# Performance work log

Hardware: AMD Instinct MI355X
Metric: run time of the kernel (lower is better)

## Reference

```python
import jax, jax.numpy as jnp
import numpy as np

NEG_SLOPE = 0.01  # F.leaky_relu default
FGW = 0.1         # feature_guidance_weight


def gat_layer(x, src, dst, W, att_l, att_r, heads, out_ch, concat):
    N = x.shape[0]
    # reward-based guidance weights (L1-normalized over nodes, F.normalize p=1 dim=0)
    rw = 1.0 / (jnp.abs(x[:, -1:]) + 1e-6)                    # [N,1]
    rw = rw / jnp.maximum(jnp.sum(jnp.abs(rw), axis=0), 1e-12)
    h = (x @ W).reshape(N, heads, out_ch)                      # [N,H,C]
    # per-node attention halves, gathered per edge (avoids [E,H,C] for scores)
    al = jnp.sum(h * att_l, axis=-1)                           # [N,H] (x_i side)
    ar = jnp.sum(h * att_r, axis=-1)                           # [N,H] (x_j side)
    alpha = jax.nn.leaky_relu(al[dst] + ar[src], NEG_SLOPE)    # [E,H]
    alpha = alpha + FGW * jnp.log(rw[src])                     # guidance from source node
    # segment softmax over incoming edges of each target node (PyG softmax)
    m = jax.ops.segment_max(alpha, dst, num_segments=N)        # [N,H]
    e = jnp.exp(alpha - m[dst])
    s = jax.ops.segment_sum(e, dst, num_segments=N)
    alpha = e / (s[dst] + 1e-16)                               # [E,H]
    # weighted scatter-aggregate of source features
    msg = h[src] * alpha[:, :, None]                           # [E,H,C]
    out = jax.ops.segment_sum(msg, dst, num_segments=N)        # [N,H,C]
    if concat:
        return out.reshape(N, heads * out_ch)
    return out.mean(axis=1)


def setup_inputs() -> dict:
    key = jax.random.key(0)
    ks = jax.random.split(key, 10)
    N, E, D_IN, HID, HEADS, D_OUT = 50000, 800000, 128, 64, 4, 1

    def xavier(k, shape, fan_in, fan_out):
        a = jnp.sqrt(6.0 / (fan_in + fan_out))
        return jax.random.uniform(k, shape, jnp.float32, -a, a)

    x = jax.random.normal(ks[0], (N, D_IN), jnp.float32)
    edge_index = jax.random.randint(ks[1], (2, E), 0, N, jnp.int32)
    W1 = xavier(ks[2], (D_IN, HEADS * HID), D_IN, HEADS * HID)
    att_l1 = xavier(ks[3], (1, HEADS, HID), HID, HID)
    att_r1 = xavier(ks[4], (1, HEADS, HID), HID, HID)
    W2 = xavier(ks[5], (HEADS * HID, HID), HEADS * HID, HID)
    att_l2 = xavier(ks[6], (1, 1, HID), HID, HID)
    att_r2 = xavier(ks[7], (1, 1, HID), HID, HID)
    fc_w = xavier(ks[8], (HID, D_OUT), HID, D_OUT)
    fc_b = jnp.zeros((D_OUT,), jnp.float32)
    return {"x": x, "edge_index": edge_index, "W1": W1, "att_l1": att_l1,
            "att_r1": att_r1, "W2": W2, "att_l2": att_l2, "att_r2": att_r2,
            "fc_w": fc_w, "fc_b": fc_b}


def reference(x, edge_index, W1, att_l1, att_r1, W2, att_l2, att_r2, fc_w, fc_b):
    src, dst = edge_index[0], edge_index[1]
    HID, HEADS = 64, 4
    h = gat_layer(x, src, dst, W1, att_l1, att_r1, HEADS, HID, concat=True)
    h = jax.nn.elu(h)  # dropout omitted (eval mode)
    h = gat_layer(h, src, dst, W2, att_l2, att_r2, 1, HID, concat=False)
    h = jax.nn.elu(h)
    return h @ fc_w + fc_b
```

## Files before the change

kernel.cpp:

```cpp
#include <hip/hip_runtime.h>
#include <hip/hip_bf16.h>

typedef __hip_bfloat16 bf16;
typedef __attribute__((ext_vector_type(8))) short bf16x8;
typedef __attribute__((ext_vector_type(4))) float f32x4;

#define NEG_SLOPE 0.01f
#define FGW 0.1f

__device__ __forceinline__ float b2f(bf16 v) { return __bfloat162float(v); }

__device__ __forceinline__ float ldf(const void* p, size_t i, int isbf) {
    return isbf ? b2f(((const bf16*)p)[i]) : ((const float*)p)[i];
}

__device__ __forceinline__ float bu2f(unsigned short u) {
    return __uint_as_float(((unsigned)u) << 16);
}
__device__ __forceinline__ unsigned short f2bu(float f) {
    return __bfloat16_as_ushort(__float2bfloat16(f));
}

__device__ __forceinline__ float waveReduceSum(float v) {
#pragma unroll
    for (int o = 32; o > 0; o >>= 1) v += __shfl_down(v, o, 64);
    return v;
}

#define ATOMIC_ADD_F32(p, v) unsafeAtomicAdd((p), (v))

__global__ __launch_bounds__(256) void k_degdet(const int* __restrict__ ei, int* __restrict__ deg, int E,
                                                const unsigned short* __restrict__ xr,
                                                float* __restrict__ sscal, int* __restrict__ flag,
                                                const void* __restrict__ W1, const void* __restrict__ W2,
                                                unsigned short* __restrict__ Wp1h,
                                                unsigned short* __restrict__ Wp1l,
                                                unsigned short* __restrict__ Wp2) {
    __shared__ int sflag;
    const int t = threadIdx.x;
    const bool packer = (blockIdx.x < 128);
    if (packer) {
        if (t < 64) {
            int big = 0;
            for (int i = t; i < 256; i += 64) {
                int ex = (xr[i] >> 7) & 0xFF;
                if (ex >= 0xBF) big = 1;
            }
            unsigned long long mk = __ballot(big);
            if (t == 0) sflag = (mk == 0ull) ? 1 : 0;
        }
        __syncthreads();
        const int isbf = sflag;
        if (blockIdx.x == 0 && t == 0) {
            *flag = isbf;
            sscal[0] = 0.f; sscal[1] = 0.f;
        }
        int id = blockIdx.x * 256 + t;
        {
            int j = id & 7, l = (id >> 3) & 63, ko = (id >> 9) & 3, T = id >> 11;
            int k = ko * 32 + (l >> 4) * 8 + j, col = T * 16 + (l & 15);
            float wv = ldf(W1, (size_t)k * 256 + col, isbf);
            unsigned short hi = f2bu(wv);
            Wp1h[id] = hi;
            Wp1l[id] = f2bu(wv - bu2f(hi));
        }
        if (id < 16384) {
            int j = id & 7, l = (id >> 3) & 63, ko = (id >> 9) & 7, T = id >> 12;
            int k = ko * 32 + (l >> 4) * 8 + j, col = T * 16 + (l & 15);
            Wp2[id] = f2bu(ldf(W2, (size_t)k * 64 + col, isbf));
        }
    }
    int e = blockIdx.x * 256 + t;
    if (e < E) atomicAdd(&deg[ei[E + e]], 1);
}

__global__ __launch_bounds__(256) void k_scanA(const int* __restrict__ deg, int* __restrict__ tmp,
                                               int* __restrict__ bsum, int N) {
    __shared__ int part[256];
    const int t = threadIdx.x;
    int i = blockIdx.x * 256 + t;
    int v = (i < N) ? ((deg[i] + 3) & ~3) : 0;
    part[t] = v;
    __syncthreads();
    for (int o = 1; o < 256; o <<= 1) {
        int add = (t >= o) ? part[t - o] : 0;
        __syncthreads();
        part[t] += add;
        __syncthreads();
    }
    if (i < N) tmp[i] = part[t];
    if (t == 255) bsum[blockIdx.x] = part[255];
}

__global__ __launch_bounds__(256) void k_scanB(int* __restrict__ bsum, int nb, int* __restrict__ rowptrN) {
    __shared__ int part[256];
    const int t = threadIdx.x;
    const int K = (nb + 255) / 256;
    int vs[8];
    int lsum = 0;
#pragma unroll
    for (int k = 0; k < 8; k++) {
        int idx = t * K + k;
        vs[k] = (k < K && idx < nb) ? bsum[idx] : 0;
        lsum += vs[k];
    }
    part[t] = lsum;
    __syncthreads();
    for (int o = 1; o < 256; o <<= 1) {
        int add = (t >= o) ? part[t - o] : 0;
        __syncthreads();
        part[t] += add;
        __syncthreads();
    }
    int excl = part[t] - lsum;
#pragma unroll
    for (int k = 0; k < 8; k++) {
        int idx = t * K + k;
        if (k < K && idx < nb) { bsum[idx] = excl; excl += vs[k]; }
    }
    if (t == 255) *rowptrN = part[255];
}

__global__ __launch_bounds__(256) void k_scanC(const int* __restrict__ deg, const int* __restrict__ tmp,
                                               const int* __restrict__ bsum, int* __restrict__ rowptr,
                                               int* __restrict__ cursor, int* __restrict__ csr_src, int N) {
    int i = blockIdx.x * 256 + threadIdx.x;
    if (i >= N) return;
    int dg = deg[i];
    int pd = (dg + 3) & ~3;
    int base = bsum[blockIdx.x] + tmp[i] - pd;
    rowptr[i] = base;
    cursor[i] = 0;
    for (int j = dg; j < pd; j++) csr_src[base + j] = N;
}

__global__ __launch_bounds__(256) void k_scatter(const int* __restrict__ ei, const int* __restrict__ rowptr,
                                                 int* __restrict__ cursor, int* __restrict__ csr_src, int E) {
    int e = blockIdx.x * 256 + threadIdx.x;
    if (e >= E) return;
    int d = ei[E + e];
    int pos = atomicAdd(&cursor[d], 1);
    csr_src[rowptr[d] + pos] = ei[e];
}

__global__ __launch_bounds__(256) void k_gemm1f(const void* __restrict__ x,
                                                const unsigned short* __restrict__ Wp1h,
                                                const unsigned short* __restrict__ Wp1l,
                                                const void* __restrict__ attl,
                                                const void* __restrict__ attr,
                                                unsigned short* __restrict__ h1,
                                                float* __restrict__ pk1,
                                                float* __restrict__ al1,
                                                float* __restrict__ rwS,
                                                int N, const int* __restrict__ flag) {
    const int isbf = *flag;
    __shared__ unsigned short Ash[64 * 136];
    __shared__ unsigned short Asl[64 * 136];
    __shared__ float rpart[64];
    const int row0 = blockIdx.x * 64;
    const int t = threadIdx.x;
    const int w = t >> 6, lane = t & 63;
    const int m = lane & 15, quad = lane >> 4;

    if (blockIdx.x == 0) {
        if (t < 32) *reinterpret_cast<uint4*>(&h1[(size_t)N * 256 + t * 8]) = (uint4){0u, 0u, 0u, 0u};
        if (t < 8) pk1[(size_t)N * 8 + t] = (t < 4) ? -1e30f : 0.f;
    }

#pragma unroll
    for (int it = 0; it < 4; it++) {
        int idx = it * 256 + t;
        int r = idx >> 4, c = idx & 15;
        if (isbf) {
            uint4 raw = {0u, 0u, 0u, 0u};
            if (row0 + r < N) {
                const unsigned short* xu = (const unsigned short*)x;
                raw = *reinterpret_cast<const uint4*>(xu + (size_t)(row0 + r) * 128 + c * 8);
            }
            *reinterpret_cast<uint4*>(&Ash[r * 136 + c * 8]) = raw;
        } else {
            float v[8];
            if (row0 + r < N) {
                const float* xf = (const float*)x;
                float4 a = *reinterpret_cast<const float4*>(xf + (size_t)(row0 + r) * 128 + c * 8);
                float4 b = *reinterpret_cast<const float4*>(xf + (size_t)(row0 + r) * 128 + c * 8 + 4);
                v[0] = a.x; v[1] = a.y; v[2] = a.z; v[3] = a.w;
                v[4] = b.x; v[5] = b.y; v[6] = b.z; v[7] = b.w;
            } else {
#pragma unroll
                for (int k = 0; k < 8; k++) v[k] = 0.f;
            }
            unsigned short hi[8], lo[8];
#pragma unroll
            for (int k = 0; k < 8; k++) {
                hi[k] = f2bu(v[k]);
                lo[k] = f2bu(v[k] - bu2f(hi[k]));
            }
            *reinterpret_cast<uint4*>(&Ash[r * 136 + c * 8]) = *reinterpret_cast<const uint4*>(hi);
            *reinterpret_cast<uint4*>(&Asl[r * 136 + c * 8]) = *reinterpret_cast<const uint4*>(lo);
        }
    }
    __syncthreads();

    bf16x8 Bh[4][4];
#pragma unroll
    for (int tt = 0; tt < 4; tt++)
#pragma unroll
        for (int ko = 0; ko < 4; ko++)
            Bh[tt][ko] = *reinterpret_cast<const bf16x8*>(
                &Wp1h[(size_t)(((w * 4 + tt) * 4 + ko) * 64 + lane) * 8]);
    float avl[4], avr[4];
#pragma unroll
    for (int tt = 0; tt < 4; tt++) {
        int col = (w * 4 + tt) * 16 + m;
        avl[tt] = ldf(attl, col, isbf);
        avr[tt] = ldf(attr, col, isbf);
    }
    for (int sub = 0; sub < 4; sub++) {
        const int rbase = sub * 16;
        bf16x8 Ah[4];
#pragma unroll
        for (int ko = 0; ko < 4; ko++)
            Ah[ko] = *reinterpret_cast<const bf16x8*>(&Ash[(rbase + m) * 136 + ko * 32 + quad * 8]);
        f32x4 Cf[4];
#pragma unroll
        for (int tt = 0; tt < 4; tt++) Cf[tt] = (f32x4){0.f, 0.f, 0.f, 0.f};
        if (isbf) {
#pragma unroll
            for (int ko = 0; ko < 4; ko++)
#pragma unroll
                for (int tt = 0; tt < 4; tt++)
                    Cf[tt] = __builtin_amdgcn_mfma_f32_16x16x32_bf16(Ah[ko], Bh[tt][ko], Cf[tt], 0, 0, 0);
        } else {
            bf16x8 Al[4];
#pragma unroll
            for (int ko = 0; ko < 4; ko++)
                Al[ko] = *reinterpret_cast<const bf16x8*>(&Asl[(rbase + m) * 136 + ko * 32 + quad * 8]);
#pragma unroll
            for (int ko = 0; ko < 4; ko++)
#pragma unroll
                for (int tt = 0; tt < 4; tt++) {
                    Cf[tt] = __builtin_amdgcn_mfma_f32_16x16x32_bf16(Ah[ko], Bh[tt][ko], Cf[tt], 0, 0, 0);
                    Cf[tt] = __builtin_amdgcn_mfma_f32_16x16x32_bf16(Al[ko], Bh[tt][ko], Cf[tt], 0, 0, 0);
                    bf16x8 Bl = *reinterpret_cast<const bf16x8*>(
                        &Wp1l[(size_t)(((w * 4 + tt) * 4 + ko) * 64 + lane) * 8]);
                    Cf[tt] = __builtin_amdgcn_mfma_f32_16x16x32_bf16(Ah[ko], Bl, Cf[tt], 0, 0, 0);
                }
        }
#pragma unroll
        for (int tt = 0; tt < 4; tt++) {
            int col = (w * 4 + tt) * 16 + m;
#pragma unroll
            for (int reg = 0; reg < 4; reg++) {
                int row = row0 + rbase + quad * 4 + reg;
                if (row < N) h1[(size_t)row * 256 + col] = f2bu(Cf[tt][reg]);
            }
        }
        if (w == 3 && m == 15) {
#pragma unroll
            for (int reg = 0; reg < 4; reg++) {
                int row = row0 + rbase + quad * 4 + reg;
                if (row < N) pk1[(size_t)row * 8 + 5] = Cf[3][reg];
            }
        }
        float sl[4], sr[4];
#pragma unroll
        for (int reg = 0; reg < 4; reg++) {
            float a = 0.f, b = 0.f;
#pragma unroll
            for (int tt = 0; tt < 4; tt++) {
                a = fmaf(avl[tt], Cf[tt][reg], a);
                b = fmaf(avr[tt], Cf[tt][reg], b);
            }
            sl[reg] = a; sr[reg] = b;
        }
#pragma unroll
        for (int off = 8; off >= 1; off >>= 1) {
#pragma unroll
            for (int reg = 0; reg < 4; reg++) {
                sl[reg] += __shfl_down(sl[reg], off, 64);
                sr[reg] += __shfl_down(sr[reg], off, 64);
            }
        }
        if (m == 0) {
#pragma unroll
            for (int reg = 0; reg < 4; reg++) {
                int row = row0 + rbase + quad * 4 + reg;
                if (row < N) {
                    al1[(size_t)row * 4 + w] = sl[reg];
                    pk1[(size_t)row * 8 + w] = sr[reg];
                }
            }
        }
    }
    if (t < 64) {
        int row = row0 + t;
        float rr = 0.f;
        if (row < N) {
            float a = fabsf(ldf(x, (size_t)row * 128 + 127, isbf));
            rr = 1.f / (a + 1e-6f);
            pk1[(size_t)row * 8 + 4] = logf(rr);
        }
        rpart[t] = rr;
    }
    __syncthreads();
    if (t == 0) {
        float s = 0.f;
#pragma unroll
        for (int i = 0; i < 64; i++) s += rpart[i];
        ATOMIC_ADD_F32(rwS, s);
    }
}

__global__ __launch_bounds__(256) void k_agg1(const int* __restrict__ rowptr,
                                              const int* __restrict__ csr_src,
                                              const float* __restrict__ al1,
                                              const float* __restrict__ pk1,
                                              const float* __restrict__ rwS,
                                              const unsigned short* __restrict__ h1,
                                              unsigned short* __restrict__ x2b,
                                              float* __restrict__ x2c, int N) {
    const int d = blockIdx.x * 4 + (threadIdx.x >> 6);
    if (d >= N) return;
    const int lane = threadIdx.x & 63;
    const int q = lane & 15;
    const int g = lane >> 4;
    const int h = q >> 2;
    const bool last15 = (q == 15);
    const float gl = FGW * logf(fmaxf(*rwS, 1e-12f));
    const unsigned qo = (unsigned)q * 32u;
    const unsigned ho4 = (unsigned)h * 4u;
    const char* pk1c = (const char*)pk1;
    const char* h1c  = (const char*)h1;

    const float al_h = al1[(size_t)d * 4 + h];
    const int beg = rowptr[d], end = rowptr[d + 1];

    float acc[16];
#pragma unroll
    for (int k = 0; k < 16; k++) acc[k] = 0.f;
    float ssum = 0.f;

    for (int base = beg; base < end; base += 32) {
        const int nst = min(end - base, 32) >> 2;

        int sj[8];
#pragma unroll
        for (int k = 0; k < 8; k++)
            if (k < nst) sj[k] = csr_src[base + k * 4 + g];

        float arP[6]; float2 lcP[6]; uint4 h0P[6], h1P[6];

#define LD1(K) do {                                                                   \
        int s_ = sj[(K)];                                                             \
        unsigned po_ = (unsigned)s_ * 32u;                                            \
        arP[(K) % 6] = *reinterpret_cast<const float*>(pk1c + po_ + ho4);             \
        lcP[(K) % 6] = *reinterpret_cast<const float2*>(pk1c + po_ + 16u);            \
        unsigned ho_ = (unsigned)s_ * 512u + qo;                                      \
        h0P[(K) % 6] = *reinterpret_cast<const uint4*>(h1c + ho_);                    \
        h1P[(K) % 6] = *reinterpret_cast<const uint4*>(h1c + ho_ + 16u);              \
    } while (0)

#define CONS1(K) do {                                                                 \
        float a_ = al_h + arP[(K) % 6];                                               \
        a_ = fmaxf(a_, NEG_SLOPE * a_);                                               \
        a_ = fmaf(FGW, lcP[(K) % 6].x, a_ - gl);                                      \
        float e_ = __expf(a_);                                                        \
        ssum += e_;                                                                   \
        uint4 cb0_ = h0P[(K) % 6], cb1_ = h1P[(K) % 6];                               \
        unsigned uu_; float lo_, hi_;                                                 \
        uu_ = cb0_.x; lo_ = __uint_as_float(uu_ << 16); hi_ = __uint_as_float(uu_ & 0xFFFF0000u); \
        acc[0] = fmaf(e_, lo_, acc[0]);  acc[1] = fmaf(e_, hi_, acc[1]);              \
        uu_ = cb0_.y; lo_ = __uint_as_float(uu_ << 16); hi_ = __uint_as_float(uu_ & 0xFFFF0000u); \
        acc[2] = fmaf(e_, lo_, acc[2]);  acc[3] = fmaf(e_, hi_, acc[3]);              \
        uu_ = cb0_.z; lo_ = __uint_as_float(uu_ << 16); hi_ = __uint_as_float(uu_ & 0xFFFF0000u); \
        acc[4] = fmaf(e_, lo_, acc[4]);  acc[5] = fmaf(e_, hi_, acc[5]);              \
        uu_ = cb0_.w; lo_ = __uint_as_float(uu_ << 16); hi_ = __uint_as_float(uu_ & 0xFFFF0000u); \
        acc[6] = fmaf(e_, lo_, acc[6]);  acc[7] = fmaf(e_, hi_, acc[7]);              \
        uu_ = cb1_.x; lo_ = __uint_as_float(uu_ << 16); hi_ = __uint_as_float(uu_ & 0xFFFF0000u); \
        acc[8] = fmaf(e_, lo_, acc[8]);  acc[9] = fmaf(e_, hi_, acc[9]);              \
        uu_ = cb1_.y; lo_ = __uint_as_float(uu_ << 16); hi_ = __uint_as_float(uu_ & 0xFFFF0000u); \
        acc[10] = fmaf(e_, lo_, acc[10]); acc[11] = fmaf(e_, hi_, acc[11]);           \
        uu_ = cb1_.z; lo_ = __uint_as_float(uu_ << 16); hi_ = __uint_as_float(uu_ & 0xFFFF0000u); \
        acc[12] = fmaf(e_, lo_, acc[12]); acc[13] = fmaf(e_, hi_, acc[13]);           \
        uu_ = cb1_.w; lo_ = __uint_as_float(uu_ << 16); hi_ = __uint_as_float(uu_ & 0xFFFF0000u); \
        hi_ = last15 ? lcP[(K) % 6].y : hi_;    \
        acc[14] = fmaf(e_, lo_, acc[14]); acc[15] = fmaf(e_, hi_, acc[15]);           \
    } while (0)

        LD1(0);
        if (1 < nst) LD1(1);
        if (2 < nst) LD1(2);
        if (3 < nst) LD1(3);
        if (4 < nst) LD1(4);
#pragma unroll
        for (int k = 0; k < 8; k++) {
            if (k >= nst) break;
            if (k + 5 < 8) { if (k + 5 < nst) LD1(k + 5); }
            CONS1(k);
        }
#undef LD1
#undef CONS1
    }

#pragma unroll
    for (int k = 0; k < 16; k++) {
        acc[k] += __shfl_xor(acc[k], 16, 64);
        acc[k] += __shfl_xor(acc[k], 32, 64);
    }
    ssum += __shfl_xor(ssum, 16, 64);
    ssum += __shfl_xor(ssum, 32, 64);

    const float inv = 1.f / (ssum + 1e-16f);
    float o0 = (g == 0 ? acc[0] : g == 1 ? acc[4]  : g == 2 ? acc[8]  : acc[12]);
    float o1 = (g == 0 ? acc[1] : g == 1 ? acc[5]  : g == 2 ? acc[9]  : acc[13]);
    float o2 = (g == 0 ? acc[2] : g == 1 ? acc[6]  : g == 2 ? acc[10] : acc[14]);
    float o3 = (g == 0 ? acc[3] : g == 1 ? acc[7]  : g == 2 ? acc[11] : acc[15]);
    o0 *= inv; o1 *= inv; o2 *= inv; o3 *= inv;
    o0 = (o0 > 0.f) ? o0 : expm1f(o0);
    o1 = (o1 > 0.f) ? o1 : expm1f(o1);
    o2 = (o2 > 0.f) ? o2 : expm1f(o2);
    o3 = (o3 > 0.f) ? o3 : expm1f(o3);
    uint2 ob;
    ob.x = (unsigned)f2bu(o0) | ((unsigned)f2bu(o1) << 16);
    ob.y = (unsigned)f2bu(o2) | ((unsigned)f2bu(o3) << 16);
    *reinterpret_cast<uint2*>(&x2b[(size_t)d * 256 + q * 16 + g * 4]) = ob;
    if (lane == 63) x2c[d] = o3;
}

__global__ __launch_bounds__(256) void k_gemm2f(const unsigned short* __restrict__ x2b,
                                                const float* __restrict__ x2c,
                                                const unsigned short* __restrict__ Wp2,
                                                const void* __restrict__ attl,
                                                const void* __restrict__ attr,
                                                unsigned short* __restrict__ h2,
                                                float* __restrict__ pk2,
                                                float* __restrict__ al2,
                                                float* __restrict__ rwS2,
                                                int N, const int* __restrict__ flag) {
    const int isbf = *flag;
    __shared__ unsigned short As[64 * 264];
    __shared__ float pl[4 * 64], pr[4 * 64], rpart[64];
    const int row0 = blockIdx.x * 64;
    const int t = threadIdx.x;
    const int w = t >> 6, lane = t & 63;
    const int m = lane & 15, quad = lane >> 4;

    if (blockIdx.x == 0) {
        if (t < 8) *reinterpret_cast<uint4*>(&h2[(size_t)N * 64 + t * 8]) = (uint4){0u, 0u, 0u, 0u};
        if (t == 0) { pk2[(size_t)N * 2] = -1e30f; pk2[(size_t)N * 2 + 1] = 0.f; }
    }

#pragma unroll
    for (int it = 0; it < 8; it++) {
        int idx = it * 256 + t;
        int r = idx >> 5, c = idx & 31;
        uint4 v = {0u, 0u, 0u, 0u};
        if (row0 + r < N)
            v = *reinterpret_cast<const uint4*>(x2b + (size_t)(row0 + r) * 256 + c * 8);
        *reinterpret_cast<uint4*>(&As[r * 264 + c * 8]) = v;
    }
    __syncthreads();
    bf16x8 Bf[8];
#pragma unroll
    for (int ko = 0; ko < 8; ko++)
        Bf[ko] = *reinterpret_cast<const bf16x8*>(&Wp2[(size_t)((w * 8 + ko) * 64 + lane) * 8]);
    f32x4 Cf[4];
#pragma unroll
    for (int sub = 0; sub < 4; sub++) Cf[sub] = (f32x4){0.f, 0.f, 0.f, 0.f};
#pragma unroll
    for (int ko = 0; ko < 8; ko++)
#pragma unroll
        for (int sub = 0; sub < 4; sub++) {
            bf16x8 Af = *reinterpret_cast<const bf16x8*>(
                &As[(sub * 16 + m) * 264 + ko * 32 + quad * 8]);
            Cf[sub] = __builtin_amdgcn_mfma_f32_16x16x32_bf16(Af, Bf[ko], Cf[sub], 0, 0, 0);
        }
    int col = w * 16 + m;
    float avl = ldf(attl, col, isbf);
    float avr = ldf(attr, col, isbf);
#pragma unroll
    for (int sub = 0; sub < 4; sub++) {
#pragma unroll
        for (int reg = 0; reg < 4; reg++) {
            int row = row0 + sub * 16 + quad * 4 + reg;
            if (row < N) h2[(size_t)row * 64 + col] = f2bu(Cf[sub][reg]);
        }
        float sl[4], sr[4];
#pragma unroll
        for (int reg = 0; reg < 4; reg++) { sl[reg] = avl * Cf[sub][reg]; sr[reg] = avr * Cf[sub][reg]; }
#pragma unroll
        for (int off = 8; off >= 1; off >>= 1) {
#pragma unroll
            for (int reg = 0; reg < 4; reg++) {
                sl[reg] += __shfl_down(sl[reg], off, 64);
                sr[reg] += __shfl_down(sr[reg], off, 64);
            }
        }
        if (m == 0) {
#pragma unroll
            for (int reg = 0; reg < 4; reg++) {
                pl[sub * 64 + w * 16 + quad * 4 + reg] = sl[reg];
                pr[sub * 64 + w * 16 + quad * 4 + reg] = sr[reg];
            }
        }
    }
    __syncthreads();
    if (t < 64) {
        int row = row0 + t;
        int sub = t >> 4, ri = t & 15;
        float rr = 0.f;
        if (row < N) {
            al2[row] = pl[sub * 64 + ri] + pl[sub * 64 + 16 + ri] + pl[sub * 64 + 32 + ri] + pl[sub * 64 + 48 + ri];
            pk2[(size_t)row * 2] = pr[sub * 64 + ri] + pr[sub * 64 + 16 + ri] + pr[sub * 64 + 32 + ri] + pr[sub * 64 + 48 + ri];
            float a = fabsf(x2c[row]);
            rr = 1.f / (a + 1e-6f);
            pk2[(size_t)row * 2 + 1] = logf(rr);
        }
        rpart[t] = rr;
    }
    __syncthreads();
    if (t == 0) {
        float s = 0.f;
#pragma unroll
        for (int i = 0; i < 64; i++) s += rpart[i];
        ATOMIC_ADD_F32(rwS2, s);
    }
}

__global__ __launch_bounds__(256) void k_agg2(const int* __restrict__ rowptr,
                                              const int* __restrict__ csr_src,
                                              const float* __restrict__ al2,
                                              const float* __restrict__ pk2,
                                              const float* __restrict__ rwS2,
                                              const unsigned short* __restrict__ h2,
                                              const void* __restrict__ fcw,
                                              const void* __restrict__ fcb,
                                              void* __restrict__ y, int N,
                                              const int* __restrict__ flag) {
    const int isbf = *flag;
    const int d = blockIdx.x * 4 + (threadIdx.x >> 6);
    if (d >= N) return;
    const int lane = threadIdx.x & 63;
    const int q = lane & 15;
    const int g = lane >> 4;
    const float gl2 = FGW * logf(fmaxf(*rwS2, 1e-12f));
    const char* pk2c = (const char*)pk2;
    const char* h2c  = (const char*)h2;
    const unsigned qo8 = (unsigned)q * 8u;

    const float al_d = al2[d];
    const int beg = rowptr[d], end = rowptr[d + 1];

    float acc[4];
#pragma unroll
    for (int k = 0; k < 4; k++) acc[k] = 0.f;
    float ssum = 0.f;

    for (int base = beg; base < end; base += 32) {
        const int nst = min(end - base, 32) >> 2;

        int sj[8];
#pragma unroll
        for (int k = 0; k < 8; k++)
            if (k < nst) sj[k] = csr_src[base + k * 4 + g];

        float2 pvP[4]; uint2 hbP[4];

#define LD2(K) do {                                                                    \
        int s_ = sj[(K)];                                                              \
        pvP[(K) & 3] = *reinterpret_cast<const float2*>(pk2c + (unsigned)s_ * 8u);     \
        hbP[(K) & 3] = *reinterpret_cast<const uint2*>(h2c + (unsigned)s_ * 128u + qo8); \
    } while (0)

#define CONS2(K) do {                                                                  \
        float a_ = al_d + pvP[(K) & 3].x;                                              \
        a_ = fmaxf(a_, NEG_SLOPE * a_);                                                \
        a_ = fmaf(FGW, pvP[(K) & 3].y, a_ - gl2);                                      \
        float e_ = __expf(a_);                                                         \
        ssum += e_;                                                                    \
        unsigned uu_ = hbP[(K) & 3].x;                                                 \
        acc[0] = fmaf(e_, __uint_as_float(uu_ << 16), acc[0]);                         \
        acc[1] = fmaf(e_, __uint_as_float(uu_ & 0xFFFF0000u), acc[1]);                 \
        uu_ = hbP[(K) & 3].y;                                                          \
        acc[2] = fmaf(e_, __uint_as_float(uu_ << 16), acc[2]);                         \
        acc[3] = fmaf(e_, __uint_as_float(uu_ & 0xFFFF0000u), acc[3]);                 \
    } while (0)

        LD2(0);
        if (1 < nst) LD2(1);
        if (2 < nst) LD2(2);
#pragma unroll
        for (int k = 0; k < 8; k++) {
            if (k >= nst) break;
            if (k + 3 < 8) { if (k + 3 < nst) LD2(k + 3); }
            CONS2(k);
        }
#undef LD2
#undef CONS2
    }

#pragma unroll
    for (int k = 0; k < 4; k++) {
        acc[k] += __shfl_xor(acc[k], 16, 64);
        acc[k] += __shfl_xor(acc[k], 32, 64);
    }
    ssum += __shfl_xor(ssum, 16, 64);
    ssum += __shfl_xor(ssum, 32, 64);

    float v = (g == 0 ? acc[0] : g == 1 ? acc[1] : g == 2 ? acc[2] : acc[3]) / (ssum + 1e-16f);
    v = (v > 0.f) ? v : expm1f(v);
    float r = waveReduceSum(v * ldf(fcw, q * 4 + g, isbf));
    if (lane == 0) {
        float o = r + ldf(fcb, 0, isbf);
        if (isbf) ((bf16*)y)[d] = __float2bfloat16(o);
        else      ((float*)y)[d] = o;
    }
}

extern "C" void kernel_launch(void* const* d_in, const int* in_sizes, int n_in,
                              void* d_out, int out_size, void* d_ws, size_t ws_size,
                              hipStream_t stream) {
    const void* x     = d_in[0];
    const int*  ei    = (const int*)d_in[1];
    const void* W1    = d_in[2];
    const void* attl1 = d_in[3];
    const void* attr1 = d_in[4];
    const void* W2    = d_in[5];
    const void* attl2 = d_in[6];
    const void* attr2 = d_in[7];
    const void* fcw   = d_in[8];
    const void* fcb   = d_in[9];

    const int N = in_sizes[0] / 128;
    const int E = in_sizes[1] / 2;
    const int NB = (N + 255) / 256;
    const int E2 = E + 4 * N;

    float* p = (float*)d_ws;
    unsigned short* h1 = (unsigned short*)p; p += (size_t)(N + 1) * 128;
    float* pk1    = p; p += (size_t)(N + 1) * 8;
    float* al1    = p; p += (size_t)N * 4;
    unsigned short* x2b = (unsigned short*)p; p += (size_t)N * 128;
    float* x2c    = p; p += (size_t)N;
    float* pk2    = p; p += (size_t)(N + 1) * 2;
    float* al2    = p; p += (size_t)N;
    int* rowptr   = (int*)p; p += (size_t)N + 1;
    int* deg      = (int*)p; p += (size_t)N;
    int* cursor   = (int*)p; p += (size_t)N;
    int* stmp     = (int*)p; p += (size_t)N;
    int* bsum     = (int*)p; p += (size_t)NB;
    int* csr_src  = (int*)p; p += (size_t)E2;
    p = (float*)(((uintptr_t)p + 15) & ~(uintptr_t)15);
    unsigned short* Wp1h = (unsigned short*)p; p += 16384;
    unsigned short* Wp1l = (unsigned short*)p; p += 16384;
    unsigned short* Wp2  = (unsigned short*)p; p += 8192;
    float* sscal  = p; p += 4;
    int* dflag = (int*)(sscal + 2);

    unsigned short* h2 = h1;

    hipMemsetAsync(deg, 0, (size_t)N * 4, stream);

    k_degdet<<<(E + 255) / 256, 256, 0, stream>>>(ei, deg, E, (const unsigned short*)x, sscal, dflag,
                                                  W1, W2, Wp1h, Wp1l, Wp2);
    k_scanA<<<NB, 256, 0, stream>>>(deg, stmp, bsum, N);
    k_scanB<<<1, 256, 0, stream>>>(bsum, NB, &rowptr[N]);
    k_scanC<<<NB, 256, 0, stream>>>(deg, stmp, bsum, rowptr, cursor, csr_src, N);
    k_scatter<<<(E + 255) / 256, 256, 0, stream>>>(ei, rowptr, cursor, csr_src, E);

    k_gemm1f<<<(N + 63) / 64, 256, 0, stream>>>(x, Wp1h, Wp1l, attl1, attr1, h1, pk1, al1,
                                                &sscal[0], N, dflag);
    k_agg1<<<(N + 3) / 4, 256, 0, stream>>>(rowptr, csr_src, al1, pk1,
                                            &sscal[0], h1, x2b, x2c, N);

    k_gemm2f<<<(N + 63) / 64, 256, 0, stream>>>(x2b, x2c, Wp2, attl2, attr2, h2, pk2, al2,
                                                &sscal[1], N, dflag);
    k_agg2<<<(N + 3) / 4, 256, 0, stream>>>(rowptr, csr_src, al2, pk2,
                                            &sscal[1], h2, fcw, fcb, d_out, N, dflag);
}
```

Measured before the change: 329.4 us.

## Fuse layer-1 aggregation with layer-2 GEMM via shared-memory tile

Merges the layer-1 edge aggregation kernel and the layer-2 projection GEMM into one 1024-thread kernel. Each of 16 waves aggregates one destination node, writes the ELU'd bf16 row into LDS, and the first four waves then run MFMA on that 16-row tile to produce h2, the attention halves and the guidance sums. This removes the global round trip of the 256-wide intermediate and one kernel launch. In exchange, 12 of the 16 waves sit idle during the GEMM, the block-wide barrier waits for the slowest node, and the load-prefetch depth drops from 5 to 3 to relieve register pressure at 1024 threads.

```diff
diff --git a/kernel.cpp b/kernel.cpp
--- a/kernel.cpp
+++ b/kernel.cpp
@@ -312,17 +312,35 @@
     }
 }
 
-__global__ __launch_bounds__(256) void k_agg1(const int* __restrict__ rowptr,
-                                              const int* __restrict__ csr_src,
-                                              const float* __restrict__ al1,
-                                              const float* __restrict__ pk1,
-                                              const float* __restrict__ rwS,
-                                              const unsigned short* __restrict__ h1,
-                                              unsigned short* __restrict__ x2b,
-                                              float* __restrict__ x2c, int N) {
-    const int d = blockIdx.x * 4 + (threadIdx.x >> 6);
-    if (d >= N) return;
-    const int lane = threadIdx.x & 63;
+__global__ __launch_bounds__(1024) void k_aggm(const int* __restrict__ rowptr,
+                                               const int* __restrict__ csr_src,
+                                               const float* __restrict__ al1,
+                                               const float* __restrict__ pk1,
+                                               const float* __restrict__ rwS,
+                                               const unsigned short* __restrict__ h1,
+                                               const unsigned short* __restrict__ Wp2,
+                                               const void* __restrict__ attl,
+                                               const void* __restrict__ attr,
+                                               unsigned short* __restrict__ h2,
+                                               float* __restrict__ pk2,
+                                               float* __restrict__ al2,
+                                               float* __restrict__ rwS2,
+                                               int N, const int* __restrict__ flag) {
+    const int isbf = *flag;
+    __shared__ unsigned short X[16 * 264];
+    __shared__ float xc[16];
+    __shared__ float pl[64], pr[64], rpart[16];
+    const int t = threadIdx.x;
+    const int wv = t >> 6;
+    const int lane = t & 63;
+    const int D0 = blockIdx.x * 16;
+
+    if (blockIdx.x == 0) {
+        if (t < 8) *reinterpret_cast<uint4*>(&h2[(size_t)N * 64 + t * 8]) = (uint4){0u, 0u, 0u, 0u};
+        if (t == 0) { pk2[(size_t)N * 2] = -1e30f; pk2[(size_t)N * 2 + 1] = 0.f; }
+    }
+
+    const int d = D0 + wv;
     const int q = lane & 15;
     const int g = lane >> 4;
     const int h = q >> 2;
@@ -333,41 +351,42 @@
     const char* pk1c = (const char*)pk1;
     const char* h1c  = (const char*)h1;
 
-    const float al_h = al1[(size_t)d * 4 + h];
-    const int beg = rowptr[d], end = rowptr[d + 1];
-
-    float acc[16];
-#pragma unroll
-    for (int k = 0; k < 16; k++) acc[k] = 0.f;
-    float ssum = 0.f;
-
-    for (int base = beg; base < end; base += 32) {
-        const int nst = min(end - base, 32) >> 2;
-
-        int sj[8];
-#pragma unroll
-        for (int k = 0; k < 8; k++)
-            if (k < nst) sj[k] = csr_src[base + k * 4 + g];
-
-        float arP[6]; float2 lcP[6]; uint4 h0P[6], h1P[6];
+    if (d < N) {
+        const float al_h = al1[(size_t)d * 4 + h];
+        const int beg = rowptr[d], end = rowptr[d + 1];
+
+        float acc[16];
+#pragma unroll
+        for (int k = 0; k < 16; k++) acc[k] = 0.f;
+        float ssum = 0.f;
+
+        for (int base = beg; base < end; base += 32) {
+            const int nst = min(end - base, 32) >> 2;
+
+            int sj[8];
+#pragma unroll
+            for (int k = 0; k < 8; k++)
+                if (k < nst) sj[k] = csr_src[base + k * 4 + g];
+
+            float arP[4]; float2 lcP[4]; uint4 h0P[4], h1P[4];
 
 #define LD1(K) do {                                                                   \
         int s_ = sj[(K)];                                                             \
         unsigned po_ = (unsigned)s_ * 32u;                                            \
-        arP[(K) % 6] = *reinterpret_cast<const float*>(pk1c + po_ + ho4);             \
-        lcP[(K) % 6] = *reinterpret_cast<const float2*>(pk1c + po_ + 16u);            \
+        arP[(K) & 3] = *reinterpret_cast<const float*>(pk1c + po_ + ho4);             \
+        lcP[(K) & 3] = *reinterpret_cast<const float2*>(pk1c + po_ + 16u);            \
         unsigned ho_ = (unsigned)s_ * 512u + qo;                                      \
-        h0P[(K) % 6] = *reinterpret_cast<const uint4*>(h1c + ho_);                    \
-        h1P[(K) % 6] = *reinterpret_cast<const uint4*>(h1c + ho_ + 16u);              \
+        h0P[(K) & 3] = *reinterpret_cast<const uint4*>(h1c + ho_);                    \
+        h1P[(K) & 3] = *reinterpret_cast<const uint4*>(h1c + ho_ + 16u);              \
     } while (0)
 
 #define CONS1(K) do {                                                                 \
-        float a_ = al_h + arP[(K) % 6];                                               \
+        float a_ = al_h + arP[(K) & 3];                                               \
         a_ = fmaxf(a_, NEG_SLOPE * a_);                                               \
-        a_ = fmaf(FGW, lcP[(K) % 6].x, a_ - gl);                                      \
+        a_ = fmaf(FGW, lcP[(K) & 3].x, a_ - gl);                                      \
         float e_ = __expf(a_);                                                        \
         ssum += e_;                                                                   \
-        uint4 cb0_ = h0P[(K) % 6], cb1_ = h1P[(K) % 6];                               \
+        uint4 cb0_ = h0P[(K) & 3], cb1_ = h1P[(K) & 3];                               \
         unsigned uu_; float lo_, hi_;                                                 \
         uu_ = cb0_.x; lo_ = __uint_as_float(uu_ << 16); hi_ = __uint_as_float(uu_ & 0xFFFF0000u); \
         acc[0] = fmaf(e_, lo_, acc[0]);  acc[1] = fmaf(e_, hi_, acc[1]);              \
@@ -384,111 +403,69 @@
         uu_ = cb1_.z; lo_ = __uint_as_float(uu_ << 16); hi_ = __uint_as_float(uu_ & 0xFFFF0000u); \
         acc[12] = fmaf(e_, lo_, acc[12]); acc[13] = fmaf(e_, hi_, acc[13]);           \
         uu_ = cb1_.w; lo_ = __uint_as_float(uu_ << 16); hi_ = __uint_as_float(uu_ & 0xFFFF0000u); \
-        hi_ = last15 ? lcP[(K) % 6].y : hi_;    \
+        hi_ = last15 ? lcP[(K) & 3].y : hi_;    \
         acc[14] = fmaf(e_, lo_, acc[14]); acc[15] = fmaf(e_, hi_, acc[15]);           \
     } while (0)
 
-        LD1(0);
-        if (1 < nst) LD1(1);
-        if (2 < nst) LD1(2);
-        if (3 < nst) LD1(3);
-        if (4 < nst) LD1(4);
-#pragma unroll
-        for (int k = 0; k < 8; k++) {
-            if (k >= nst) break;
-            if (k + 5 < 8) { if (k + 5 < nst) LD1(k + 5); }
-            CONS1(k);
-        }
+            LD1(0);
+            if (1 < nst) LD1(1);
+            if (2 < nst) LD1(2);
+#pragma unroll
+            for (int k = 0; k < 8; k++) {
+                if (k >= nst) break;
+                if (k + 3 < 8) { if (k + 3 < nst) LD1(k + 3); }
+                CONS1(k);
+            }
 #undef LD1
 #undef CONS1
-    }
-
-#pragma unroll
-    for (int k = 0; k < 16; k++) {
-        acc[k] += __shfl_xor(acc[k], 16, 64);
-        acc[k] += __shfl_xor(acc[k], 32, 64);
-    }
-    ssum += __shfl_xor(ssum, 16, 64);
-    ssum += __shfl_xor(ssum, 32, 64);
-
-    const float inv = 1.f / (ssum + 1e-16f);
-    float o0 = (g == 0 ? acc[0] : g == 1 ? acc[4]  : g == 2 ? acc[8]  : acc[12]);
-    float o1 = (g == 0 ? acc[1] : g == 1 ? acc[5]  : g == 2 ? acc[9]  : acc[13]);
-    float o2 = (g == 0 ? acc[2] : g == 1 ? acc[6]  : g == 2 ? acc[10] : acc[14]);
-    float o3 = (g == 0 ? acc[3] : g == 1 ? acc[7]  : g == 2 ? acc[11] : acc[15]);
-    o0 *= inv; o1 *= inv; o2 *= inv; o3 *= inv;
-    o0 = (o0 > 0.f) ? o0 : expm1f(o0);
-    o1 = (o1 > 0.f) ? o1 : expm1f(o1);
-    o2 = (o2 > 0.f) ? o2 : expm1f(o2);
-    o3 = (o3 > 0.f) ? o3 : expm1f(o3);
-    uint2 ob;
-    ob.x = (unsigned)f2bu(o0) | ((unsigned)f2bu(o1) << 16);
-    ob.y = (unsigned)f2bu(o2) | ((unsigned)f2bu(o3) << 16);
-    *reinterpret_cast<uint2*>(&x2b[(size_t)d * 256 + q * 16 + g * 4]) = ob;
-    if (lane == 63) x2c[d] = o3;
-}
-
-__global__ __launch_bounds__(256) void k_gemm2f(const unsigned short* __restrict__ x2b,
-                                                const float* __restrict__ x2c,
-                                                const unsigned short* __restrict__ Wp2,
-                                                const void* __restrict__ attl,
-                                                const void* __restrict__ attr,
-                                                unsigned short* __restrict__ h2,
-                                                float* __restrict__ pk2,
-                                                float* __restrict__ al2,
-                                                float* __restrict__ rwS2,
-                                                int N, const int* __restrict__ flag) {
-    const int isbf = *flag;
-    __shared__ unsigned short As[64 * 264];
-    __shared__ float pl[4 * 64], pr[4 * 64], rpart[64];
-    const int row0 = blockIdx.x * 64;
-    const int t = threadIdx.x;
-    const int w = t >> 6, lane = t & 63;
+        }
+
+#pragma unroll
+        for (int k = 0; k < 16; k++) {
+            acc[k] += __shfl_xor(acc[k], 16, 64);
+            acc[k] += __shfl_xor(acc[k], 32, 64);
+        }
+        ssum += __shfl_xor(ssum, 16, 64);
+        ssum += __shfl_xor(ssum, 32, 64);
+
+        const float inv = 1.f / (ssum + 1e-16f);
+        float o0 = (g == 0 ? acc[0] : g == 1 ? acc[4]  : g == 2 ? acc[8]  : acc[12]);
+        float o1 = (g == 0 ? acc[1] : g == 1 ? acc[5]  : g == 2 ? acc[9]  : acc[13]);
+        float o2 = (g == 0 ? acc[2] : g == 1 ? acc[6]  : g == 2 ? acc[10] : acc[14]);
+        float o3 = (g == 0 ? acc[3] : g == 1 ? acc[7]  : g == 2 ? acc[11] : acc[15]);
+        o0 *= inv; o1 *= inv; o2 *= inv; o3 *= inv;
+        o0 = (o0 > 0.f) ? o0 : expm1f(o0);
+        o1 = (o1 > 0.f) ? o1 : expm1f(o1);
+        o2 = (o2 > 0.f) ? o2 : expm1f(o2);
+        o3 = (o3 > 0.f) ? o3 : expm1f(o3);
+        uint2 ob;
+        ob.x = (unsigned)f2bu(o0) | ((unsigned)f2bu(o1) << 16);
+        ob.y = (unsigned)f2bu(o2) | ((unsigned)f2bu(o3) << 16);
+        *reinterpret_cast<uint2*>(&X[wv * 264 + q * 16 + g * 4]) = ob;
+        if (lane == 63) xc[wv] = o3;
+    }
+    __syncthreads();
+
     const int m = lane & 15, quad = lane >> 4;
-
-    if (blockIdx.x == 0) {
-        if (t < 8) *reinterpret_cast<uint4*>(&h2[(size_t)N * 64 + t * 8]) = (uint4){0u, 0u, 0u, 0u};
-        if (t == 0) { pk2[(size_t)N * 2] = -1e30f; pk2[(size_t)N * 2 + 1] = 0.f; }
-    }
-
-#pragma unroll
-    for (int it = 0; it < 8; it++) {
-        int idx = it * 256 + t;
-        int r = idx >> 5, c = idx & 31;
-        uint4 v = {0u, 0u, 0u, 0u};
-        if (row0 + r < N)
-            v = *reinterpret_cast<const uint4*>(x2b + (size_t)(row0 + r) * 256 + c * 8);
-        *reinterpret_cast<uint4*>(&As[r * 264 + c * 8]) = v;
-    }
-    __syncthreads();
-    bf16x8 Bf[8];
-#pragma unroll
-    for (int ko = 0; ko < 8; ko++)
-        Bf[ko] = *reinterpret_cast<const bf16x8*>(&Wp2[(size_t)((w * 8 + ko) * 64 + lane) * 8]);
-    f32x4 Cf[4];
-#pragma unroll
-    for (int sub = 0; sub < 4; sub++) Cf[sub] = (f32x4){0.f, 0.f, 0.f, 0.f};
-#pragma unroll
-    for (int ko = 0; ko < 8; ko++)
-#pragma unroll
-        for (int sub = 0; sub < 4; sub++) {
-            bf16x8 Af = *reinterpret_cast<const bf16x8*>(
-                &As[(sub * 16 + m) * 264 + ko * 32 + quad * 8]);
-            Cf[sub] = __builtin_amdgcn_mfma_f32_16x16x32_bf16(Af, Bf[ko], Cf[sub], 0, 0, 0);
-        }
-    int col = w * 16 + m;
-    float avl = ldf(attl, col, isbf);
-    float avr = ldf(attr, col, isbf);
-#pragma unroll
-    for (int sub = 0; sub < 4; sub++) {
+    if (wv < 4) {
+        f32x4 Cf = (f32x4){0.f, 0.f, 0.f, 0.f};
+#pragma unroll
+        for (int ko = 0; ko < 8; ko++) {
+            bf16x8 Bf = *reinterpret_cast<const bf16x8*>(&Wp2[(size_t)((wv * 8 + ko) * 64 + lane) * 8]);
+            bf16x8 Af = *reinterpret_cast<const bf16x8*>(&X[m * 264 + ko * 32 + quad * 8]);
+            Cf = __builtin_amdgcn_mfma_f32_16x16x32_bf16(Af, Bf, Cf, 0, 0, 0);
+        }
+        const int col = wv * 16 + m;
+        const float avl = ldf(attl, col, isbf);
+        const float avr = ldf(attr, col, isbf);
+        float sl[4], sr[4];
 #pragma unroll
         for (int reg = 0; reg < 4; reg++) {
-            int row = row0 + sub * 16 + quad * 4 + reg;
-            if (row < N) h2[(size_t)row * 64 + col] = f2bu(Cf[sub][reg]);
-        }
-        float sl[4], sr[4];
-#pragma unroll
-        for (int reg = 0; reg < 4; reg++) { sl[reg] = avl * Cf[sub][reg]; sr[reg] = avr * Cf[sub][reg]; }
+            int row = D0 + quad * 4 + reg;
+            if (row < N) h2[(size_t)row * 64 + col] = f2bu(Cf[reg]);
+            sl[reg] = avl * Cf[reg];
+            sr[reg] = avr * Cf[reg];
+        }
 #pragma unroll
         for (int off = 8; off >= 1; off >>= 1) {
 #pragma unroll
@@ -500,20 +477,19 @@
         if (m == 0) {
 #pragma unroll
             for (int reg = 0; reg < 4; reg++) {
-                pl[sub * 64 + w * 16 + quad * 4 + reg] = sl[reg];
-                pr[sub * 64 + w * 16 + quad * 4 + reg] = sr[reg];
+                pl[wv * 16 + quad * 4 + reg] = sl[reg];
+                pr[wv * 16 + quad * 4 + reg] = sr[reg];
             }
         }
     }
     __syncthreads();
-    if (t < 64) {
-        int row = row0 + t;
-        int sub = t >> 4, ri = t & 15;
+    if (t < 16) {
+        int row = D0 + t;
         float rr = 0.f;
         if (row < N) {
-            al2[row] = pl[sub * 64 + ri] + pl[sub * 64 + 16 + ri] + pl[sub * 64 + 32 + ri] + pl[sub * 64 + 48 + ri];
-            pk2[(size_t)row * 2] = pr[sub * 64 + ri] + pr[sub * 64 + 16 + ri] + pr[sub * 64 + 32 + ri] + pr[sub * 64 + 48 + ri];
-            float a = fabsf(x2c[row]);
+            al2[row] = pl[t] + pl[16 + t] + pl[32 + t] + pl[48 + t];
+            pk2[(size_t)row * 2] = pr[t] + pr[16 + t] + pr[32 + t] + pr[48 + t];
+            float a = fabsf(xc[t]);
             rr = 1.f / (a + 1e-6f);
             pk2[(size_t)row * 2 + 1] = logf(rr);
         }
@@ -523,7 +499,7 @@
     if (t == 0) {
         float s = 0.f;
 #pragma unroll
-        for (int i = 0; i < 64; i++) s += rpart[i];
+        for (int i = 0; i < 16; i++) s += rpart[i];
         ATOMIC_ADD_F32(rwS2, s);
     }
 }
@@ -657,8 +633,9 @@
     unsigned short* Wp2  = (unsigned short*)p; p += 8192;
     float* sscal  = p; p += 4;
     int* dflag = (int*)(sscal + 2);
-
-    unsigned short* h2 = h1;
+    (void)x2c;
+
+    unsigned short* h2 = x2b;
 
     hipMemsetAsync(deg, 0, (size_t)N * 4, stream);
 
@@ -671,11 +648,11 @@
 
     k_gemm1f<<<(N + 63) / 64, 256, 0, stream>>>(x, Wp1h, Wp1l, attl1, attr1, h1, pk1, al1,
                                                 &sscal[0], N, dflag);
-    k_agg1<<<(N + 3) / 4, 256, 0, stream>>>(rowptr, csr_src, al1, pk1,
-                                            &sscal[0], h1, x2b, x2c, N);
-
-    k_gemm2f<<<(N + 63) / 64, 256, 0, stream>>>(x2b, x2c, Wp2, attl2, attr2, h2, pk2, al2,
-                                                &sscal[1], N, dflag);
+
+    k_aggm<<<(N + 15) / 16, 1024, 0, stream>>>(rowptr, csr_src, al1, pk1, &sscal[0], h1,
+                                               Wp2, attl2, attr2, h2, pk2, al2,
+                                               &sscal[1], N, dflag);
+
     k_agg2<<<(N + 3) / 4, 256, 0, stream>>>(rowptr, csr_src, al2, pk2,
                                             &sscal[1], h2, fcw, fcb, d_out, N, dflag);
 }
```

Result: slower. 381.2 us (+15.7%).
